# Optimization experiments

Measured on AMD Instinct MI355X. Metric: run time of the kernel, lower is better.

Reference implementation:

```python
import jax, jax.numpy as jnp
import numpy as np

H = 4           # attention heads
NEG_SLOPE = 0.2 # GATConv default leaky_relu slope
BN_EPS = 1e-5


def gat_conv(x, src, dst, W, a_src, a_dst, b, N):
    # PyG GATConv (concat=True, add_self_loops=True): self-loops appended by caller.
    C = W.shape[1] // H
    h = (x @ W).reshape(N, H, C)                      # [N,H,C]
    al_s = jnp.einsum('nhc,hc->nh', h, a_src)          # [N,H]
    al_d = jnp.einsum('nhc,hc->nh', h, a_dst)
    e = jax.nn.leaky_relu(al_s[src] + al_d[dst], NEG_SLOPE)   # [E,H]
    m = jax.ops.segment_max(e, dst, num_segments=N)            # per-dst softmax (stable)
    p = jnp.exp(e - m[dst])
    s = jax.ops.segment_sum(p, dst, num_segments=N)
    alpha = p / s[dst]                                          # [E,H]
    out = jax.ops.segment_sum(alpha[:, :, None] * h[src], dst, num_segments=N)  # [N,H,C]
    return out.reshape(N, H * C) + b


def mp_layer(x, src, dst, gw, gas, gad, gb, fw, fb, fg, fbeta, N):
    gat_out = gat_conv(x, src, dst, gw, gas, gad, gb, N)
    # feature_transform: Linear -> BatchNorm1d (eval: running_mean=0, running_var=1) -> ReLU
    y = x @ fw + fb
    y = y * (fg / jnp.sqrt(1.0 + BN_EPS)) + fbeta
    y = jax.nn.relu(y)
    return gat_out + y


def forward(x, edge_index, edge_attr, params):
    N = x.shape[0]
    loop = jnp.arange(N, dtype=edge_index.dtype)
    src = jnp.concatenate([edge_index[0], loop])   # add self loops (GATConv default)
    dst = jnp.concatenate([edge_index[1], loop])
    for p in params[:-1]:
        x = mp_layer(x, src, dst, *p, N)
        x = jax.nn.relu(x)   # dropout is identity in eval mode
    cw, cb = params[-1]
    return x @ cw + cb


def setup_inputs() -> dict:
    N, E, D, Hd, O = 80000, 1000000, 512, 128, 10
    key = jax.random.key(0)
    ks = jax.random.split(key, 40)
    ki = iter(range(40))

    def rn(shape, fan_in):
        return jax.random.normal(ks[next(ki)], shape, dtype=jnp.float32) / np.sqrt(fan_in)

    inp = {}
    inp['x'] = jax.random.normal(ks[next(ki)], (N, D), dtype=jnp.float32)
    inp['edge_index'] = jax.random.randint(ks[next(ki)], (2, E), 0, N, dtype=jnp.int64)
    inp['edge_attr'] = jax.random.uniform(ks[next(ki)], (E, 1), dtype=jnp.float32)
    dims = [D, Hd, Hd]
    for li, din in enumerate(dims):
        inp[f'l{li}_gw'] = rn((din, Hd), din)
        inp[f'l{li}_gas'] = rn((H, Hd // H), Hd // H)
        inp[f'l{li}_gad'] = rn((H, Hd // H), Hd // H)
        inp[f'l{li}_gb'] = jnp.zeros((Hd,), jnp.float32)
        inp[f'l{li}_fw'] = rn((din, Hd), din)
        inp[f'l{li}_fb'] = jnp.zeros((Hd,), jnp.float32)
        inp[f'l{li}_fg'] = jnp.ones((Hd,), jnp.float32)
        inp[f'l{li}_fbeta'] = jnp.zeros((Hd,), jnp.float32)
    inp['cls_w'] = rn((Hd, O), Hd)
    inp['cls_b'] = jnp.zeros((O,), jnp.float32)
    return inp


def reference(x, edge_index, edge_attr,
              l0_gw, l0_gas, l0_gad, l0_gb, l0_fw, l0_fb, l0_fg, l0_fbeta,
              l1_gw, l1_gas, l1_gad, l1_gb, l1_fw, l1_fb, l1_fg, l1_fbeta,
              l2_gw, l2_gas, l2_gad, l2_gb, l2_fw, l2_fb, l2_fg, l2_fbeta,
              cls_w, cls_b):
    params = [
        (l0_gw, l0_gas, l0_gad, l0_gb, l0_fw, l0_fb, l0_fg, l0_fbeta),
        (l1_gw, l1_gas, l1_gad, l1_gb, l1_fw, l1_fb, l1_fg, l1_fbeta),
        (l2_gw, l2_gas, l2_gad, l2_gb, l2_fw, l2_fb, l2_fg, l2_fbeta),
        (cls_w, cls_b),
    ]
    return forward(x, edge_index, edge_attr, params)
```

## Files before the change

### kernel.cpp

```cpp
#include <hip/hip_runtime.h>
#include <cstdint>
#include <cstddef>

#define HD 128
#define NEG_SLOPE 0.2f
#define BN_EPS 1e-5f

typedef __bf16 bf16x8 __attribute__((ext_vector_type(8)));
typedef float  f32x4  __attribute__((ext_vector_type(4)));

__device__ __forceinline__ unsigned short f2b(float f) {
    unsigned int u = __float_as_uint(f);
    u = (u + 0x7fffu + ((u >> 16) & 1u)) >> 16;
    return (unsigned short)u;
}
__device__ __forceinline__ unsigned int pack2(float lo, float hi) {
    return (unsigned int)f2b(lo) | ((unsigned int)f2b(hi) << 16);
}

__device__ __forceinline__ void gload_lds16(const void* g, void* l) {
    __builtin_amdgcn_global_load_lds(
        (const __attribute__((address_space(1))) uint32_t*)g,
        (__attribute__((address_space(3))) uint32_t*)l, 16, 0, 0);
}

__global__ void prep_w2(const float* __restrict__ gw, const float* __restrict__ fw,
                        unsigned short* __restrict__ Wt, int K)
{
    int t = blockIdx.x * 256 + threadIdx.x;
    if (t >= K * 256) return;
    int k = t >> 8, c = t & 255;
    float v = (c < 128) ? gw[(size_t)k * 128 + c] : fw[(size_t)k * 128 + (c - 128)];
    Wt[(size_t)c * K + k] = f2b(v);
}

#define WAITV4 asm volatile("s_waitcnt vmcnt(4)" ::: "memory");
#define WAITV0 asm volatile("s_waitcnt vmcnt(0)" ::: "memory");
#define BAR    __builtin_amdgcn_s_barrier();

#define STAGE(BUF, KOFF)                                                      \
    _Pragma("unroll") for (int i = 0; i < 2; i++)                             \
        gload_lds16(ap[i] + (KOFF), (BUF) + (w + i * 8) * 1024);              \
    _Pragma("unroll") for (int i = 0; i < 2; i++)                             \
        gload_lds16(bp[i] + (KOFF), (BUF) + 16384 + (w + i * 8) * 1024);

#define COMPUTE(BUF)                                                          \
    {                                                                         \
        bf16x8 af[4], bfr[4];                                                 \
        _Pragma("unroll") for (int rt = 0; rt < 4; rt++) {                    \
            int arow = 64 * wm + rt * 16 + m;                                 \
            const char* base = (BUF) + (arow << 7);                           \
            int sw = (m & 7) << 4;                                            \
            f32x4 a0 = *(const f32x4*)(base + ((q * 32)      ^ sw));          \
            f32x4 a1 = *(const f32x4*)(base + ((q * 32 + 16) ^ sw));          \
            uint4 av;                                                         \
            av.x = pack2(a0.x, a0.y); av.y = pack2(a0.z, a0.w);               \
            av.z = pack2(a1.x, a1.y); av.w = pack2(a1.z, a1.w);               \
            af[rt] = *(bf16x8*)&av;                                           \
        }                                                                     \
        _Pragma("unroll") for (int ct = 0; ct < 4; ct++) {                    \
            int brow = 64 * wn + ct * 16 + m;                                 \
            bfr[ct] = *(const bf16x8*)((BUF) + 16384 + (brow << 6) +          \
                                       ((q * 16) ^ (((m >> 1) & 3) << 4)));   \
        }                                                                     \
        _Pragma("unroll") for (int rt = 0; rt < 4; rt++)                      \
            _Pragma("unroll") for (int ct = 0; ct < 4; ct++)                  \
                acc[rt][ct] = __builtin_amdgcn_mfma_f32_16x16x32_bf16(        \
                    af[rt], bfr[ct], acc[rt][ct], 0, 0, 0);                   \
    }

__global__ __launch_bounds__(512, 4) void gemm_dual(
    const float* __restrict__ X, const unsigned short* __restrict__ Wt,
    unsigned short* __restrict__ hb, float* __restrict__ yb, int M, int K,
    const float* __restrict__ fb, const float* __restrict__ fg,
    const float* __restrict__ fbeta, const float* __restrict__ gb)
{
    __shared__ __align__(16) char smem[2 * 32768];
    char* buf0 = smem;
    char* buf1 = smem + 32768;

    const int tid  = threadIdx.x;
    const int row0 = blockIdx.x * 128;
    const int w    = tid >> 6, lane = tid & 63;
    const int wm   = w & 1,  wn = w >> 1;
    const int m    = lane & 15, q = lane >> 4;

    const int la = lane >> 3, ca = lane & 7;
    const int lb = lane >> 2, cb = lane & 3;
    const int oA = 4 * (ca ^ la);
    const int oB = 8 * (cb ^ (la & 3));

    const float* ap[2];
    const unsigned short* bp[2];
#pragma unroll
    for (int i = 0; i < 2; i++) {
        int ch = w + i * 8;
        int gr = row0 + ch * 8 + la; if (gr >= M) gr = M - 1;
        ap[i] = X + (size_t)gr * K + oA;
        int rB = ch * 16 + lb;
        bp[i] = Wt + (size_t)rB * K + oB;
    }

    f32x4 acc[4][4];
#pragma unroll
    for (int rt = 0; rt < 4; rt++)
#pragma unroll
        for (int ct = 0; ct < 4; ct++) acc[rt][ct] = (f32x4){0.f, 0.f, 0.f, 0.f};

    STAGE(buf0, 0)
    for (int ks = 0; ks < K; ks += 64) {
        STAGE(buf1, ks + 32)
        WAITV4
        BAR
        COMPUTE(buf0)
        BAR
        if (ks + 64 < K) { STAGE(buf0, ks + 64) WAITV4 } else { WAITV0 }
        BAR
        COMPUTE(buf1)
        BAR
    }

    const bool full = (row0 + 128 <= M);
    if (wn < 2) {
#pragma unroll
        for (int ct = 0; ct < 4; ct++) {
            int col = 64 * wn + ct * 16 + m;
#pragma unroll
            for (int rt = 0; rt < 4; rt++)
#pragma unroll
                for (int r = 0; r < 4; r++) {
                    int row = row0 + 64 * wm + rt * 16 + q * 4 + r;
                    if (full || row < M) hb[(size_t)row * HD + col] = f2b(acc[rt][ct][r]);
                }
        }
    } else {
        const float inv_bn = 1.0f / sqrtf(1.0f + BN_EPS);
#pragma unroll
        for (int ct = 0; ct < 4; ct++) {
            int col = 64 * (wn - 2) + ct * 16 + m;
            float g  = fg[col] * inv_bn;
            float bb = fb[col];
            float bt = fbeta[col];
            float gv = gb[col];
#pragma unroll
            for (int rt = 0; rt < 4; rt++)
#pragma unroll
                for (int r = 0; r < 4; r++) {
                    int row = row0 + 64 * wm + rt * 16 + q * 4 + r;
                    if (full || row < M) {
                        float y = (acc[rt][ct][r] + bb) * g + bt;
                        y = y > 0.f ? y : 0.f;
                        yb[(size_t)row * HD + col] = y + gv;
                    }
                }
        }
    }
}

__global__ void al_kernel(const unsigned short* __restrict__ h,
                          const float* __restrict__ a_src, const float* __restrict__ a_dst,
                          float* __restrict__ als, float* __restrict__ ald, int N)
{
    int t = blockIdx.x * blockDim.x + threadIdx.x;
    if (t >= N * 4) return;
    int n = t >> 2, hd = t & 3;
    const unsigned short* hp = h + (size_t)n * HD + hd * 32;
    const float* as = a_src + hd * 32;
    const float* ad = a_dst + hd * 32;
    float s1 = 0.f, s2 = 0.f;
#pragma unroll
    for (int i = 0; i < 32; i += 8) {
        uint4 hv = *(const uint4*)(hp + i);
        unsigned int u[4] = {hv.x, hv.y, hv.z, hv.w};
#pragma unroll
        for (int p = 0; p < 4; p++) {
            float f0 = __uint_as_float(u[p] << 16);
            float f1 = __uint_as_float(u[p] & 0xffff0000u);
            s1 += f0 * as[i + 2 * p] + f1 * as[i + 2 * p + 1];
            s2 += f0 * ad[i + 2 * p] + f1 * ad[i + 2 * p + 1];
        }
    }
    als[t] = s1; ald[t] = s2;
}

__global__ void hist_kernel(const int* __restrict__ ei, int E, int N, int* __restrict__ deg)
{
    int t = blockIdx.x * blockDim.x + threadIdx.x;
    if (t >= E + N) return;
    int d = (t < E) ? ei[E + t] : (t - E);
    atomicAdd(&deg[d], 1);
}

__global__ void scan1(const int* __restrict__ deg, int* __restrict__ rp,
                      int* __restrict__ bsum, int N)
{
    __shared__ int sh[256];
    int t = threadIdx.x;
    int i0 = blockIdx.x * 1024 + t * 4;
    int v[4];
#pragma unroll
    for (int j = 0; j < 4; j++) v[j] = (i0 + j < N) ? deg[i0 + j] : 0;
    int tot = v[0] + v[1] + v[2] + v[3];
    sh[t] = tot;
    __syncthreads();
    for (int off = 1; off < 256; off <<= 1) {
        int xv = (t >= off) ? sh[t - off] : 0;
        __syncthreads();
        sh[t] += xv;
        __syncthreads();
    }
    int run = sh[t] - tot;
    if (t == 255) bsum[blockIdx.x] = sh[255];
#pragma unroll
    for (int j = 0; j < 4; j++) {
        if (i0 + j < N) rp[i0 + j] = run;
        run += v[j];
    }
}

__global__ void scan2(int* __restrict__ bsum, int nb)
{
    if (threadIdx.x == 0 && blockIdx.x == 0) {
        int run = 0;
        for (int i = 0; i < nb; i++) { int v = bsum[i]; bsum[i] = run; run += v; }
    }
}

__global__ void scan3(int* __restrict__ rp, int* __restrict__ cur,
                      const int* __restrict__ bsum, int N, int Etot)
{
    int t = blockIdx.x * blockDim.x + threadIdx.x;
    if (t < N) {
        int v = rp[t] + bsum[t >> 10];
        rp[t] = v;
        cur[t] = v;
    } else if (t == N) {
        rp[N] = Etot;
    }
}

__global__ void scatter_kernel(const int* __restrict__ ei, int E, int N,
                               int* __restrict__ cur, int* __restrict__ col)
{
    int t = blockIdx.x * blockDim.x + threadIdx.x;
    if (t >= E + N) return;
    int s, d;
    if (t < E) { s = ei[t]; d = ei[E + t]; } else { s = t - E; d = t - E; }
    int p = atomicAdd(&cur[d], 1);
    col[p] = s;
}

__global__ __launch_bounds__(256) void agg_kernel(
    const unsigned short* __restrict__ h, const float* __restrict__ als,
    const float* __restrict__ ald, const int* __restrict__ rp,
    const int* __restrict__ col, float* __restrict__ xio, int N)
{
    int wid  = (blockIdx.x * blockDim.x + threadIdx.x) >> 6;
    int lane = threadIdx.x & 63;
    if (wid >= N) return;
    int beg = rp[wid], end = rp[wid + 1];

    int g = lane >> 4, c = lane & 15, hB = c >> 2;
    float ad_h = ald[wid * 4 + hB];
    float acc[8];
#pragma unroll
    for (int p = 0; p < 8; p++) acc[p] = 0.f;
    float wsum = 0.f;
    const unsigned short* hbase = h + c * 8;

    int j = beg + g;
    float alc = 0.f;
    uint4 hvc = (uint4){0, 0, 0, 0};
    if (j < end) {
        int s0 = col[j];
        alc = als[s0 * 4 + hB];
        hvc = *(const uint4*)(hbase + (size_t)s0 * HD);
    }
    while (j < end) {
        int jn = j + 4;
        float aln = 0.f;
        uint4 hvn = (uint4){0, 0, 0, 0};
        if (jn < end) {
            int sn = col[jn];
            aln = als[sn * 4 + hB];
            hvn = *(const uint4*)(hbase + (size_t)sn * HD);
        }
        float e = alc + ad_h;
        e = e > 0.f ? e : NEG_SLOPE * e;
        float wgt = __expf(e);
        wsum += wgt;
        unsigned int uu[4] = {hvc.x, hvc.y, hvc.z, hvc.w};
#pragma unroll
        for (int p = 0; p < 4; p++) {
            acc[2 * p]     += wgt * __uint_as_float(uu[p] << 16);
            acc[2 * p + 1] += wgt * __uint_as_float(uu[p] & 0xffff0000u);
        }
        j = jn; alc = aln; hvc = hvn;
    }
#pragma unroll
    for (int p = 0; p < 8; p++) {
        acc[p] += __shfl_xor(acc[p], 16);
        acc[p] += __shfl_xor(acc[p], 32);
    }
    wsum += __shfl_xor(wsum, 16);
    wsum += __shfl_xor(wsum, 32);
    if (g == 0) {
        float inv = 1.0f / wsum;
        float* xp = xio + (size_t)wid * HD + c * 8;
        float4 x0 = *(float4*)xp, x1 = *(float4*)(xp + 4);
        float o[8] = {acc[0] * inv + x0.x, acc[1] * inv + x0.y,
                      acc[2] * inv + x0.z, acc[3] * inv + x0.w,
                      acc[4] * inv + x1.x, acc[5] * inv + x1.y,
                      acc[6] * inv + x1.z, acc[7] * inv + x1.w};
#pragma unroll
        for (int p = 0; p < 8; p++) o[p] = o[p] > 0.f ? o[p] : 0.f;
        *(float4*)xp       = (float4){o[0], o[1], o[2], o[3]};
        *(float4*)(xp + 4) = (float4){o[4], o[5], o[6], o[7]};
    }
}

__global__ __launch_bounds__(256) void cls_kernel(
    const float* __restrict__ x, const float* __restrict__ w,
    const float* __restrict__ b, float* __restrict__ out, int N)
{
    int wid  = (blockIdx.x * blockDim.x + threadIdx.x) >> 6;
    int lane = threadIdx.x & 63;
    if (wid >= N) return;
    float x0 = x[(size_t)wid * HD + lane];
    float x1 = x[(size_t)wid * HD + 64 + lane];
    float acc[10];
#pragma unroll
    for (int o = 0; o < 10; o++)
        acc[o] = x0 * w[lane * 10 + o] + x1 * w[(lane + 64) * 10 + o];
#pragma unroll
    for (int o = 0; o < 10; o++) {
        float v = acc[o];
#pragma unroll
        for (int off = 1; off < 64; off <<= 1) v += __shfl_xor(v, off);
        acc[o] = v;
    }
    float v = 0.f;
#pragma unroll
    for (int o = 0; o < 10; o++) if (lane == o) v = acc[o];
    if (lane < 10) out[(size_t)wid * 10 + lane] = v + b[lane];
}

extern "C" void kernel_launch(void* const* d_in, const int* in_sizes, int n_in,
                              void* d_out, int out_size, void* d_ws, size_t ws_size,
                              hipStream_t stream)
{
    const float* x0 = (const float*)d_in[0];
    const int*   ei = (const int*)d_in[1];
    const int N = in_sizes[0] / 512;
    const int E = in_sizes[1] / 2;
    const int Etot = E + N;

    const float *gw[3], *gas[3], *gad[3], *gbp[3], *fw[3], *fbp[3], *fgp[3], *fbt[3];
    for (int l = 0; l < 3; l++) {
        int b = 3 + 8 * l;
        gw[l]  = (const float*)d_in[b + 0];
        gas[l] = (const float*)d_in[b + 1];
        gad[l] = (const float*)d_in[b + 2];
        gbp[l] = (const float*)d_in[b + 3];
        fw[l]  = (const float*)d_in[b + 4];
        fbp[l] = (const float*)d_in[b + 5];
        fgp[l] = (const float*)d_in[b + 6];
        fbt[l] = (const float*)d_in[b + 7];
    }
    const float* cw = (const float*)d_in[27];
    const float* cb = (const float*)d_in[28];

    char* p = (char*)d_ws;
    auto carve = [&](size_t bytes) -> char* {
        char* r = p; p += (bytes + 255) & ~(size_t)255; return r;
    };
    float* xA   = (float*)carve((size_t)N * HD * 4);
    float* xB   = (float*)carve((size_t)N * HD * 4);
    unsigned short* hbuf = (unsigned short*)carve((size_t)N * HD * 2);
    float* als  = (float*)carve((size_t)N * 4 * 4);
    float* ald  = (float*)carve((size_t)N * 4 * 4);
    int* rp   = (int*)carve((size_t)(N + 1) * 4);
    int* deg  = (int*)carve((size_t)N * 4);
    int* cur  = (int*)carve((size_t)N * 4);
    int* bsum = (int*)carve(4096);
    int* col  = (int*)carve((size_t)Etot * 4);
    unsigned short* wT[3];
    for (int l = 0; l < 3; l++) {
        int K = (l == 0) ? 512 : HD;
        wT[l] = (unsigned short*)carve((size_t)256 * K * 2);
    }

    for (int l = 0; l < 3; l++) {
        int K = (l == 0) ? 512 : HD;
        int nt = K * 256;
        prep_w2<<<(nt + 255) / 256, 256, 0, stream>>>(gw[l], fw[l], wT[l], K);
    }

    hipMemsetAsync(deg, 0, (size_t)N * 4, stream);
    hist_kernel<<<(Etot + 255) / 256, 256, 0, stream>>>(ei, E, N, deg);
    int nb = (N + 1023) / 1024;
    scan1<<<nb, 256, 0, stream>>>(deg, rp, bsum, N);
    scan2<<<1, 64, 0, stream>>>(bsum, nb);
    scan3<<<(N + 256) / 256, 256, 0, stream>>>(rp, cur, bsum, N, Etot);
    scatter_kernel<<<(Etot + 255) / 256, 256, 0, stream>>>(ei, E, N, cur, col);

    for (int l = 0; l < 3; l++) {
        const float* xin = (l == 0) ? x0 : ((l == 1) ? xA : xB);
        float* xout = (l == 1) ? xB : xA;
        int K = (l == 0) ? 512 : HD;
        int mblocks = (N + 127) / 128;
        gemm_dual<<<mblocks, 512, 0, stream>>>(xin, wT[l], hbuf, xout, N, K,
                                               fbp[l], fgp[l], fbt[l], gbp[l]);
        al_kernel<<<(N * 4 + 255) / 256, 256, 0, stream>>>(hbuf, gas[l], gad[l], als, ald, N);
        agg_kernel<<<(N + 3) / 4, 256, 0, stream>>>(hbuf, als, ald, rp, col, xout, N);
    }

    cls_kernel<<<(N + 3) / 4, 256, 0, stream>>>(xA, cw, cb, (float*)d_out, N);
}
```

Measured before the change: 770.8 us.

## Fuse attention logits into GEMM epilogue and classifier into aggregation

Attention logits (als/ald) are now computed in the GEMM epilogue from fp32 accumulators using shuffle reductions, which removes the separate al_kernel and its re-read of h. The final classifier is folded into the last layer's aggregation kernel, so the layer-3 output is never written and re-read. The aggregation kernel also changes from 4 to 8 edges in flight per wave, with 16 features per lane. The trade-offs are more epilogue shuffles, higher register pressure in agg, and logits now taken from fp32 values instead of bf16-rounded h.

```diff
diff --git a/kernel.cpp b/kernel.cpp
--- a/kernel.cpp
+++ b/kernel.cpp
@@ -73,7 +73,9 @@
     const float* __restrict__ X, const unsigned short* __restrict__ Wt,
     unsigned short* __restrict__ hb, float* __restrict__ yb, int M, int K,
     const float* __restrict__ fb, const float* __restrict__ fg,
-    const float* __restrict__ fbeta, const float* __restrict__ gb)
+    const float* __restrict__ fbeta, const float* __restrict__ gb,
+    const float* __restrict__ a_src, const float* __restrict__ a_dst,
+    float* __restrict__ als, float* __restrict__ ald)
 {
     __shared__ __align__(16) char smem[2 * 32768];
     char* buf0 = smem;
@@ -133,6 +135,34 @@
                     if (full || row < M) hb[(size_t)row * HD + col] = f2b(acc[rt][ct][r]);
                 }
         }
+        const int hA = 2 * wn, hB2 = 2 * wn + 1;
+        const float asA0 = a_src[hA * 32 + m],  asA1 = a_src[hA * 32 + 16 + m];
+        const float asB0 = a_src[hB2 * 32 + m], asB1 = a_src[hB2 * 32 + 16 + m];
+        const float adA0 = a_dst[hA * 32 + m],  adA1 = a_dst[hA * 32 + 16 + m];
+        const float adB0 = a_dst[hB2 * 32 + m], adB1 = a_dst[hB2 * 32 + 16 + m];
+#pragma unroll
+        for (int rt = 0; rt < 4; rt++)
+#pragma unroll
+            for (int r = 0; r < 4; r++) {
+                int row = row0 + 64 * wm + rt * 16 + q * 4 + r;
+                float sA = acc[rt][0][r] * asA0 + acc[rt][1][r] * asA1;
+                float sB = acc[rt][2][r] * asB0 + acc[rt][3][r] * asB1;
+                float dA = acc[rt][0][r] * adA0 + acc[rt][1][r] * adA1;
+                float dB = acc[rt][2][r] * adB0 + acc[rt][3][r] * adB1;
+#pragma unroll
+                for (int off = 1; off < 16; off <<= 1) {
+                    sA += __shfl_xor(sA, off);
+                    sB += __shfl_xor(sB, off);
+                    dA += __shfl_xor(dA, off);
+                    dB += __shfl_xor(dB, off);
+                }
+                if (m == 0 && (full || row < M)) {
+                    als[row * 4 + hA]  = sA;
+                    als[row * 4 + hB2] = sB;
+                    ald[row * 4 + hA]  = dA;
+                    ald[row * 4 + hB2] = dB;
+                }
+            }
     } else {
         const float inv_bn = 1.0f / sqrtf(1.0f + BN_EPS);
 #pragma unroll
@@ -155,32 +185,6 @@
                 }
         }
     }
-}
-
-__global__ void al_kernel(const unsigned short* __restrict__ h,
-                          const float* __restrict__ a_src, const float* __restrict__ a_dst,
-                          float* __restrict__ als, float* __restrict__ ald, int N)
-{
-    int t = blockIdx.x * blockDim.x + threadIdx.x;
-    if (t >= N * 4) return;
-    int n = t >> 2, hd = t & 3;
-    const unsigned short* hp = h + (size_t)n * HD + hd * 32;
-    const float* as = a_src + hd * 32;
-    const float* ad = a_dst + hd * 32;
-    float s1 = 0.f, s2 = 0.f;
-#pragma unroll
-    for (int i = 0; i < 32; i += 8) {
-        uint4 hv = *(const uint4*)(hp + i);
-        unsigned int u[4] = {hv.x, hv.y, hv.z, hv.w};
-#pragma unroll
-        for (int p = 0; p < 4; p++) {
-            float f0 = __uint_as_float(u[p] << 16);
-            float f1 = __uint_as_float(u[p] & 0xffff0000u);
-            s1 += f0 * as[i + 2 * p] + f1 * as[i + 2 * p + 1];
-            s2 += f0 * ad[i + 2 * p] + f1 * ad[i + 2 * p + 1];
-        }
-    }
-    als[t] = s1; ald[t] = s2;
 }
 
 __global__ void hist_kernel(const int* __restrict__ ei, int E, int N, int* __restrict__ deg)
@@ -253,96 +257,104 @@
 __global__ __launch_bounds__(256) void agg_kernel(
     const unsigned short* __restrict__ h, const float* __restrict__ als,
     const float* __restrict__ ald, const int* __restrict__ rp,
-    const int* __restrict__ col, float* __restrict__ xio, int N)
+    const int* __restrict__ col, float* __restrict__ xio, int N,
+    const float* __restrict__ cw, const float* __restrict__ cb,
+    float* __restrict__ out)
 {
     int wid  = (blockIdx.x * blockDim.x + threadIdx.x) >> 6;
     int lane = threadIdx.x & 63;
     if (wid >= N) return;
     int beg = rp[wid], end = rp[wid + 1];
 
-    int g = lane >> 4, c = lane & 15, hB = c >> 2;
+    int g = lane >> 3, c = lane & 7, hB = c >> 1;
     float ad_h = ald[wid * 4 + hB];
-    float acc[8];
-#pragma unroll
-    for (int p = 0; p < 8; p++) acc[p] = 0.f;
+    float acc[16];
+#pragma unroll
+    for (int p = 0; p < 16; p++) acc[p] = 0.f;
     float wsum = 0.f;
-    const unsigned short* hbase = h + c * 8;
+    const unsigned short* hbase = h + c * 16;
 
     int j = beg + g;
     float alc = 0.f;
-    uint4 hvc = (uint4){0, 0, 0, 0};
+    uint4 hvc0 = (uint4){0, 0, 0, 0}, hvc1 = (uint4){0, 0, 0, 0};
     if (j < end) {
         int s0 = col[j];
         alc = als[s0 * 4 + hB];
-        hvc = *(const uint4*)(hbase + (size_t)s0 * HD);
+        const uint4* hp = (const uint4*)(hbase + (size_t)s0 * HD);
+        hvc0 = hp[0]; hvc1 = hp[1];
     }
     while (j < end) {
-        int jn = j + 4;
+        int jn = j + 8;
         float aln = 0.f;
-        uint4 hvn = (uint4){0, 0, 0, 0};
+        uint4 hvn0 = (uint4){0, 0, 0, 0}, hvn1 = (uint4){0, 0, 0, 0};
         if (jn < end) {
             int sn = col[jn];
             aln = als[sn * 4 + hB];
-            hvn = *(const uint4*)(hbase + (size_t)sn * HD);
+            const uint4* hp = (const uint4*)(hbase + (size_t)sn * HD);
+            hvn0 = hp[0]; hvn1 = hp[1];
         }
         float e = alc + ad_h;
         e = e > 0.f ? e : NEG_SLOPE * e;
         float wgt = __expf(e);
         wsum += wgt;
-        unsigned int uu[4] = {hvc.x, hvc.y, hvc.z, hvc.w};
-#pragma unroll
-        for (int p = 0; p < 4; p++) {
+        unsigned int uu[8] = {hvc0.x, hvc0.y, hvc0.z, hvc0.w,
+                              hvc1.x, hvc1.y, hvc1.z, hvc1.w};
+#pragma unroll
+        for (int p = 0; p < 8; p++) {
             acc[2 * p]     += wgt * __uint_as_float(uu[p] << 16);
             acc[2 * p + 1] += wgt * __uint_as_float(uu[p] & 0xffff0000u);
         }
-        j = jn; alc = aln; hvc = hvn;
-    }
-#pragma unroll
-    for (int p = 0; p < 8; p++) {
+        j = jn; alc = aln; hvc0 = hvn0; hvc1 = hvn1;
+    }
+#pragma unroll
+    for (int p = 0; p < 16; p++) {
+        acc[p] += __shfl_xor(acc[p], 8);
         acc[p] += __shfl_xor(acc[p], 16);
         acc[p] += __shfl_xor(acc[p], 32);
     }
+    wsum += __shfl_xor(wsum, 8);
     wsum += __shfl_xor(wsum, 16);
     wsum += __shfl_xor(wsum, 32);
     if (g == 0) {
         float inv = 1.0f / wsum;
-        float* xp = xio + (size_t)wid * HD + c * 8;
-        float4 x0 = *(float4*)xp, x1 = *(float4*)(xp + 4);
-        float o[8] = {acc[0] * inv + x0.x, acc[1] * inv + x0.y,
-                      acc[2] * inv + x0.z, acc[3] * inv + x0.w,
-                      acc[4] * inv + x1.x, acc[5] * inv + x1.y,
-                      acc[6] * inv + x1.z, acc[7] * inv + x1.w};
-#pragma unroll
-        for (int p = 0; p < 8; p++) o[p] = o[p] > 0.f ? o[p] : 0.f;
-        *(float4*)xp       = (float4){o[0], o[1], o[2], o[3]};
-        *(float4*)(xp + 4) = (float4){o[4], o[5], o[6], o[7]};
-    }
-}
-
-__global__ __launch_bounds__(256) void cls_kernel(
-    const float* __restrict__ x, const float* __restrict__ w,
-    const float* __restrict__ b, float* __restrict__ out, int N)
-{
-    int wid  = (blockIdx.x * blockDim.x + threadIdx.x) >> 6;
-    int lane = threadIdx.x & 63;
-    if (wid >= N) return;
-    float x0 = x[(size_t)wid * HD + lane];
-    float x1 = x[(size_t)wid * HD + 64 + lane];
-    float acc[10];
-#pragma unroll
-    for (int o = 0; o < 10; o++)
-        acc[o] = x0 * w[lane * 10 + o] + x1 * w[(lane + 64) * 10 + o];
-#pragma unroll
-    for (int o = 0; o < 10; o++) {
-        float v = acc[o];
-#pragma unroll
-        for (int off = 1; off < 64; off <<= 1) v += __shfl_xor(v, off);
-        acc[o] = v;
-    }
-    float v = 0.f;
-#pragma unroll
-    for (int o = 0; o < 10; o++) if (lane == o) v = acc[o];
-    if (lane < 10) out[(size_t)wid * 10 + lane] = v + b[lane];
+        float* xp = xio + (size_t)wid * HD + c * 16;
+        float xv[16];
+#pragma unroll
+        for (int b = 0; b < 4; b++)
+            *(float4*)(xv + 4 * b) = *(const float4*)(xp + 4 * b);
+        float o_[16];
+#pragma unroll
+        for (int p = 0; p < 16; p++) {
+            float t = acc[p] * inv + xv[p];
+            o_[p] = t > 0.f ? t : 0.f;
+        }
+        if (cw == nullptr) {
+#pragma unroll
+            for (int b = 0; b < 4; b++)
+                *(float4*)(xp + 4 * b) = *(const float4*)(o_ + 4 * b);
+        } else {
+            float po[10];
+#pragma unroll
+            for (int o = 0; o < 10; o++) {
+                float s = 0.f;
+#pragma unroll
+                for (int p = 0; p < 16; p++)
+                    s += o_[p] * cw[(c * 16 + p) * 10 + o];
+                po[o] = s;
+            }
+#pragma unroll
+            for (int o = 0; o < 10; o++) {
+                po[o] += __shfl_xor(po[o], 1);
+                po[o] += __shfl_xor(po[o], 2);
+                po[o] += __shfl_xor(po[o], 4);
+            }
+            if (c == 0) {
+#pragma unroll
+                for (int o = 0; o < 10; o++)
+                    out[(size_t)wid * 10 + o] = po[o] + cb[o];
+            }
+        }
+    }
 }
 
 extern "C" void kernel_launch(void* const* d_in, const int* in_sizes, int n_in,
@@ -410,10 +422,10 @@
         int K = (l == 0) ? 512 : HD;
         int mblocks = (N + 127) / 128;
         gemm_dual<<<mblocks, 512, 0, stream>>>(xin, wT[l], hbuf, xout, N, K,
-                                               fbp[l], fgp[l], fbt[l], gbp[l]);
-        al_kernel<<<(N * 4 + 255) / 256, 256, 0, stream>>>(hbuf, gas[l], gad[l], als, ald, N);
-        agg_kernel<<<(N + 3) / 4, 256, 0, stream>>>(hbuf, als, ald, rp, col, xout, N);
-    }
-
-    cls_kernel<<<(N + 3) / 4, 256, 0, stream>>>(xA, cw, cb, (float*)d_out, N);
-}
+                                               fbp[l], fgp[l], fbt[l], gbp[l],
+                                               gas[l], gad[l], als, ald);
+        agg_kernel<<<(N + 3) / 4, 256, 0, stream>>>(
+            hbuf, als, ald, rp, col, xout, N,
+            (l == 2) ? cw : nullptr, cb, (float*)d_out);
+    }
+}
```

Result: slower. 791.6 us (+2.7%).
